# Performance work log

Hardware: AMD Instinct MI355X
Metric: run time of the kernel (lower is better)

Reference implementation:

```python
import jax, jax.numpy as jnp
import numpy as np
from jax import lax

A = 3          # anchors per scale
C = 80         # num foreground classes (COCO)
NMS_THRESH = 0.45
NMS_TOPK = 400
POST_NMS = 100


def setup_inputs() -> dict:
    key = jax.random.key(0)
    k0, k1, k2 = jax.random.split(key, 3)
    B = 8
    ch = A * (C + 5)  # 255
    # raw head outputs (pre-decode conv activations), modest scale so exp() stays sane
    tip0 = jax.random.normal(k0, (B, ch, 19, 19), jnp.float32) * 0.5
    tip1 = jax.random.normal(k1, (B, ch, 38, 38), jnp.float32) * 0.5
    tip2 = jax.random.normal(k2, (B, ch, 76, 76), jnp.float32) * 0.5
    # standard YOLOv3 COCO anchors, deepest scale (stride 32) first
    anchors0 = jnp.array([[116., 90.], [156., 198.], [373., 326.]], jnp.float32)
    anchors1 = jnp.array([[30., 61.], [62., 45.], [59., 119.]], jnp.float32)
    anchors2 = jnp.array([[10., 13.], [16., 30.], [33., 23.]], jnp.float32)
    return dict(tip0=tip0, tip1=tip1, tip2=tip2,
                anchors0=anchors0, anchors1=anchors1, anchors2=anchors2)


def _decode(tip, anchors, stride):
    """YOLOOutputV3 inference decode. tip: (B, A*(C+5), H, W)."""
    B, _, H, W = tip.shape
    # (B, A*(C+5), H*W) -> (B, H*W, A, C+5)
    pred = tip.reshape(B, A * (C + 5), H * W).transpose(0, 2, 1).reshape(B, H * W, A, C + 5)
    gx, gy = jnp.meshgrid(jnp.arange(W), jnp.arange(H))       # each (H, W)
    offsets = jnp.stack([gx, gy], -1).reshape(1, H * W, 1, 2).astype(tip.dtype)
    centers = (jax.nn.sigmoid(pred[..., :2]) + offsets) * stride          # (B,HW,A,2)
    scales = jnp.exp(pred[..., 2:4]) * anchors.reshape(1, 1, A, 2)        # (B,HW,A,2)
    conf = jax.nn.sigmoid(pred[..., 4:5])                                 # objectness
    cls_scores = jax.nn.sigmoid(pred[..., 5:]) * conf                      # (B,HW,A,C)
    wh = scales * 0.5
    bbox = jnp.concatenate([centers - wh, centers + wh], -1)               # corner format
    return bbox.reshape(B, H * W * A, 4), cls_scores.reshape(B, H * W * A, C)


def _pairwise_iou(b):
    """b: (K,4) corner boxes -> (K,K) IoU."""
    x1, y1, x2, y2 = b[:, 0], b[:, 1], b[:, 2], b[:, 3]
    area = jnp.maximum(x2 - x1, 0.) * jnp.maximum(y2 - y1, 0.)
    iw = jnp.maximum(jnp.minimum(x2[:, None], x2[None, :]) - jnp.maximum(x1[:, None], x1[None, :]), 0.)
    ih = jnp.maximum(jnp.minimum(y2[:, None], y2[None, :]) - jnp.maximum(y1[:, None], y1[None, :]), 0.)
    inter = iw * ih
    return inter / (area[:, None] + area[None, :] - inter + 1e-12)


def _nms_single(det):
    """Class-aware greedy NMS on one image. det: (M,6) = (cid, score, x1,y1,x2,y2)."""
    K = NMS_TOPK
    _, idx = lax.top_k(det[:, 1], K)     # sort by score, keep top K
    d = det[idx]                          # (K,6), descending score
    iou = _pairwise_iou(d[:, 2:6])
    same = d[:, 0][:, None] == d[:, 0][None, :]   # only same class suppresses
    valid = d[:, 1] > 0.
    rng = jnp.arange(K)

    def body(i, keep):
        sup = (iou[i] > NMS_THRESH) & same[i] & (rng > i) & keep[i] & valid[i]
        return keep & ~sup

    keep = lax.fori_loop(0, K, body, jnp.ones((K,), bool)) & valid
    d = jnp.where(keep[:, None], d, jnp.full_like(d, -1.))
    order = jnp.argsort(-d[:, 1])         # kept (sorted) first, suppressed (-1) last
    return d[order][:POST_NMS]            # (POST_NMS, 6)


def _detect(tip0, tip1, tip2, anchors0, anchors1, anchors2):
    dets = []
    for tip, anc, stride in ((tip0, anchors0, 32), (tip1, anchors1, 16), (tip2, anchors2, 8)):
        bbox, scores = _decode(tip, anc, stride)          # (B,N,4), (B,N,C)
        B, N, _ = bbox.shape
        ids = jnp.broadcast_to(jnp.arange(C, dtype=bbox.dtype)[None, None, :, None], (B, N, C, 1))
        sc = scores[..., None]                            # (B,N,C,1)
        bx = jnp.broadcast_to(bbox[:, :, None, :], (B, N, C, 4))
        dets.append(jnp.concatenate([ids, sc, bx], -1).reshape(B, N * C, 6))
    det = jnp.concatenate(dets, 1)                        # (B, M, 6)
    return jax.vmap(_nms_single)(det)                     # (B, POST_NMS, 6)


def reference(tip0, tip1, tip2, anchors0, anchors1, anchors2):
    res = _detect(tip0, tip1, tip2, anchors0, anchors1, anchors2)
    ids = res[..., 0:1]
    scores = res[..., 1:2]
    bboxes = res[..., 2:6]
    return ids, scores, bboxes
```

## Files before the change

### kernel.cpp

```cpp
#include <hip/hip_runtime.h>
#include <stdint.h>

#define NUMA 3
#define NUMC 80
#define CAP  49152
#define CAP2 8192
#define KTOP 400
#define POST 100
#define NBIN1 2048
#define EQCAP 1024
#define KEY0 0x3EE66666u
#define LBUF 2048

typedef float f32x4 __attribute__((ext_vector_type(4)));

__device__ __forceinline__ float sigmoidf_(float x) { return 1.0f / (1.0f + expf(-x)); }
__device__ __forceinline__ unsigned uminu(unsigned a, unsigned b) { return a < b ? a : b; }

__global__ void init_kernel(unsigned* __restrict__ p) {
    int i = blockIdx.x * blockDim.x + threadIdx.x;
    if (i < NBIN1 * 16 + 40) p[i] = 0;
}

__global__ __launch_bounds__(256) void score_main(
        const float* __restrict__ t0, const float* __restrict__ t1,
        const float* __restrict__ t2,
        unsigned* __restrict__ ccnt, unsigned* __restrict__ ckey,
        unsigned* __restrict__ cidx, unsigned* __restrict__ histN)
{
    __shared__ unsigned lkey[LBUF], lidx[LBUF];
    __shared__ unsigned lh[NBIN1];
    __shared__ unsigned lcnt, lbase;
    const int tid = threadIdx.x;
    if (tid == 0) lcnt = 0;
    for (int i = tid; i < NBIN1; i += 256) lh[i] = 0;
    __syncthreads();

    const int ba = blockIdx.z;
    const int b = ba / 3, a = ba - 3 * b;
    const int c0 = blockIdx.y * 8;
    const int cx = blockIdx.x;

    #define LEMIT(SC, IDX) do { \
        unsigned key_ = __float_as_uint(SC); \
        if (key_ >= KEY0) { \
            atomicAdd(&lh[(key_ - KEY0) >> 13], 1u); \
            unsigned pos_ = atomicAdd(&lcnt, 1u); \
            if (pos_ < LBUF) { lkey[pos_] = key_; lidx[pos_] = (IDX); } \
        } \
    } while (0)

    if (cx < 2) {
        const int hw = cx * 256 + tid;
        if (hw < 361) {
            const float* base = t0 + (size_t)(b * 255 + a * 85) * 361;
            float cr = base[4 * 361 + hw];
            const float* p0 = base + (size_t)(5 + c0) * 361 + hw;
            float x0 = p0[0 * 361], x1 = p0[1 * 361], x2 = p0[2 * 361], x3 = p0[3 * 361];
            float x4 = p0[4 * 361], x5 = p0[5 * 361], x6 = p0[6 * 361], x7 = p0[7 * 361];
            float cf = sigmoidf_(cr);
            unsigned ib = (unsigned)((hw * NUMA + a) * NUMC + c0);
            LEMIT(sigmoidf_(x0) * cf, ib + 0);
            LEMIT(sigmoidf_(x1) * cf, ib + 1);
            LEMIT(sigmoidf_(x2) * cf, ib + 2);
            LEMIT(sigmoidf_(x3) * cf, ib + 3);
            LEMIT(sigmoidf_(x4) * cf, ib + 4);
            LEMIT(sigmoidf_(x5) * cf, ib + 5);
            LEMIT(sigmoidf_(x6) * cf, ib + 6);
            LEMIT(sigmoidf_(x7) * cf, ib + 7);
        }
    } else {
        const float* tip; int vHW, v, candOff;
        if (cx < 4) { tip = t1; vHW = 361;  v = (cx - 2) * 256 + tid; candOff = 86640; }
        else        { tip = t2; vHW = 1444; v = (cx - 4) * 256 + tid; candOff = 433200; }
        if (v < vHW) {
            const f32x4* bp = (const f32x4*)(tip + (size_t)(b * 255 + a * 85) * (size_t)(vHW * 4));
            f32x4 cv = bp[(size_t)4 * vHW + v];
            const f32x4* p0 = bp + (size_t)(5 + c0) * vHW + v;
            f32x4 s0 = p0[0 * (size_t)vHW], s1 = p0[1 * (size_t)vHW];
            f32x4 s2 = p0[2 * (size_t)vHW], s3 = p0[3 * (size_t)vHW];
            f32x4 s4 = p0[4 * (size_t)vHW], s5 = p0[5 * (size_t)vHW];
            f32x4 s6 = p0[6 * (size_t)vHW], s7 = p0[7 * (size_t)vHW];
            float cf0 = sigmoidf_(cv[0]), cf1 = sigmoidf_(cv[1]);
            float cf2 = sigmoidf_(cv[2]), cf3 = sigmoidf_(cv[3]);
            unsigned ib0 = (unsigned)(candOff + (v * 4 * NUMA + a) * NUMC + c0);
            #define EMIT4(S, U) do { \
                unsigned ib = ib0 + (U); \
                LEMIT(sigmoidf_((S)[0]) * cf0, ib); \
                LEMIT(sigmoidf_((S)[1]) * cf1, ib + 240); \
                LEMIT(sigmoidf_((S)[2]) * cf2, ib + 480); \
                LEMIT(sigmoidf_((S)[3]) * cf3, ib + 720); \
            } while (0)
            EMIT4(s0, 0); EMIT4(s1, 1); EMIT4(s2, 2); EMIT4(s3, 3);
            EMIT4(s4, 4); EMIT4(s5, 5); EMIT4(s6, 6); EMIT4(s7, 7);
            #undef EMIT4
        }
    }
    #undef LEMIT

    __syncthreads();
    if (tid == 0) {
        unsigned c = lcnt;
        if (c > LBUF) {
            atomicOr(&ccnt[b], 0x80000000u);
            lbase = 0xFFFFFFFFu;
        } else {
            lbase = atomicAdd(&ccnt[b], c);
        }
    }
    __syncthreads();
    unsigned c = uminu(lcnt, (unsigned)LBUF);
    unsigned basep = lbase;
    if (basep != 0xFFFFFFFFu) {
        for (unsigned i = tid; i < c; i += 256) {
            unsigned p = basep + i;
            if (p < CAP) {
                ckey[(size_t)b * CAP + p] = lkey[i];
                cidx[(size_t)b * CAP + p] = lidx[i];
            }
        }
    }
    unsigned* gh = histN + b * NBIN1;
    for (int i = tid; i < NBIN1; i += 256) {
        unsigned v2 = lh[i];
        if (v2) atomicAdd(&gh[i], v2);
    }
}

__device__ __forceinline__ void wave_select(const unsigned* h, int nbins, unsigned rank,
                                            unsigned* resv, int tid)
{
    if (tid >= 64) return;
    const int lane = tid;
    const int cs = nbins >> 6;
    unsigned v = 0;
    for (int k = 0; k < cs; k++) {
        int off = (k + lane) & (cs - 1);
        v += h[lane * cs + off];
    }
    unsigned S = v;
    #pragma unroll
    for (int o = 1; o < 64; o <<= 1) {
        unsigned t = (unsigned)__shfl_down((int)S, o);
        if (lane + o < 64) S += t;
    }
    unsigned long long bm = __ballot(S >= rank);
    if (bm == 0ull) bm = 1ull;
    int C = 63 - __builtin_clzll(bm);
    unsigned SC = (unsigned)__builtin_amdgcn_readlane((int)S, C);
    unsigned vC = (unsigned)__builtin_amdgcn_readlane((int)v, C);
    unsigned rem = rank - (SC - vC);
    unsigned w = (lane < cs) ? h[C * cs + lane] : 0u;
    unsigned T = w;
    #pragma unroll
    for (int o = 1; o < 64; o <<= 1) {
        unsigned t = (unsigned)__shfl_down((int)T, o);
        if (lane + o < 64) T += t;
    }
    unsigned long long bm2 = __ballot((T >= rem) && (lane < cs));
    if (bm2 == 0ull) bm2 = 1ull;
    int B = 63 - __builtin_clzll(bm2);
    unsigned TB = (unsigned)__builtin_amdgcn_readlane((int)T, B);
    unsigned wB = (unsigned)__builtin_amdgcn_readlane((int)w, B);
    if (lane == 0) {
        resv[0] = (unsigned)(C * cs + B);
        resv[1] = rem - (TB - wB);
    }
}

__global__ __launch_bounds__(256) void findcut_v(const unsigned* __restrict__ histN,
                                                 unsigned* __restrict__ cutfloor,
                                                 unsigned* __restrict__ ccnt,
                                                 unsigned* __restrict__ flags) {
    __shared__ unsigned h[NBIN1];
    __shared__ unsigned resv[2];
    int b = blockIdx.x;
    for (int i = threadIdx.x; i < NBIN1; i += 256) h[i] = histN[b * NBIN1 + i];
    __syncthreads();
    wave_select(h, NBIN1, KTOP, resv, threadIdx.x);
    __syncthreads();
    if (threadIdx.x == 0) {
        unsigned c = ccnt[b];
        bool ok = (c >= KTOP) && (c <= CAP);
        flags[b] = ok ? 1u : 0u;
        if (ok) {
            cutfloor[b] = KEY0 + (resv[0] << 13);
        } else {
            cutfloor[b] = 0u;
            ccnt[b] = 0;
        }
    }
}

__global__ __launch_bounds__(256) void fb_hist(
        const float* __restrict__ t0, const float* __restrict__ t1,
        const float* __restrict__ t2,
        unsigned* __restrict__ histF, const unsigned* __restrict__ flags)
{
    const int ba = blockIdx.z;
    const int b = ba / 3, a = ba - 3 * b;
    if (flags[b]) return;
    __shared__ unsigned lh[NBIN1];
    const int tid = threadIdx.x;
    for (int i = tid; i < NBIN1; i += 256) lh[i] = 0;
    __syncthreads();
    const int c0 = blockIdx.y * 8;
    const int cx = blockIdx.x;
    if (cx < 2) {
        const int hw = cx * 256 + tid;
        if (hw < 361) {
            const float* base = t0 + (size_t)(b * 255 + a * 85) * 361;
            float cf = sigmoidf_(base[4 * 361 + hw]);
            for (int u = 0; u < 8; u++) {
                float sc = sigmoidf_(base[(size_t)(5 + c0 + u) * 361 + hw]) * cf;
                atomicAdd(&lh[__float_as_uint(sc) >> 19], 1u);
            }
        }
    } else {
        const float* tip; int vHW, v;
        if (cx < 4) { tip = t1; vHW = 361;  v = (cx - 2) * 256 + tid; }
        else        { tip = t2; vHW = 1444; v = (cx - 4) * 256 + tid; }
        if (v < vHW) {
            const f32x4* bp = (const f32x4*)(tip + (size_t)(b * 255 + a * 85) * (size_t)(vHW * 4));
            f32x4 cv = bp[(size_t)4 * vHW + v];
            float cf[4] = { sigmoidf_(cv[0]), sigmoidf_(cv[1]), sigmoidf_(cv[2]), sigmoidf_(cv[3]) };
            for (int u = 0; u < 8; u++) {
                f32x4 s = bp[(size_t)(5 + c0 + u) * vHW + v];
                for (int l = 0; l < 4; l++)
                    atomicAdd(&lh[__float_as_uint(sigmoidf_(s[l]) * cf[l]) >> 19], 1u);
            }
        }
    }
    __syncthreads();
    unsigned* gh = histF + b * NBIN1;
    for (int i = tid; i < NBIN1; i += 256) {
        unsigned v2 = lh[i];
        if (v2) atomicAdd(&gh[i], v2);
    }
}

__global__ __launch_bounds__(256) void fb_cut(const unsigned* __restrict__ histF,
                                              unsigned* __restrict__ cutb,
                                              const unsigned* __restrict__ flags) {
    int b = blockIdx.x;
    if (flags[b]) return;
    __shared__ unsigned h[NBIN1];
    __shared__ unsigned resv[2];
    for (int i = threadIdx.x; i < NBIN1; i += 256) h[i] = histF[b * NBIN1 + i];
    __syncthreads();
    wave_select(h, NBIN1, KTOP, resv, threadIdx.x);
    __syncthreads();
    if (threadIdx.x == 0) cutb[b] = resv[0];
}

__global__ __launch_bounds__(256) void fb_compact(
        const float* __restrict__ t0, const float* __restrict__ t1,
        const float* __restrict__ t2,
        const unsigned* __restrict__ cutb, unsigned* __restrict__ ccnt,
        unsigned* __restrict__ ckey, unsigned* __restrict__ cidx,
        const unsigned* __restrict__ flags)
{
    const int ba = blockIdx.z;
    const int b = ba / 3, a = ba - 3 * b;
    if (flags[b]) return;
    const int tid = threadIdx.x;
    const int c0 = blockIdx.y * 8;
    const int cx = blockIdx.x;
    unsigned cutkey = cutb[b] << 19;

    if (cx < 2) {
        const int hw = cx * 256 + tid;
        if (hw < 361) {
            const float* base = t0 + (size_t)(b * 255 + a * 85) * 361;
            float cf = sigmoidf_(base[4 * 361 + hw]);
            for (int u = 0; u < 8; u++) {
                float sc = sigmoidf_(base[(size_t)(5 + c0 + u) * 361 + hw]) * cf;
                unsigned key = __float_as_uint(sc);
                if (key >= cutkey) {
                    unsigned pos = atomicAdd(&ccnt[b], 1u);
                    if (pos < CAP) {
                        ckey[(size_t)b * CAP + pos] = key;
                        cidx[(size_t)b * CAP + pos] = (unsigned)((hw * NUMA + a) * NUMC + c0 + u);
                    }
                }
            }
        }
    } else {
        const float* tip; int vHW, v, candOff;
        if (cx < 4) { tip = t1; vHW = 361;  v = (cx - 2) * 256 + tid; candOff = 86640; }
        else        { tip = t2; vHW = 1444; v = (cx - 4) * 256 + tid; candOff = 433200; }
        if (v < vHW) {
            const f32x4* bp = (const f32x4*)(tip + (size_t)(b * 255 + a * 85) * (size_t)(vHW * 4));
            f32x4 cv = bp[(size_t)4 * vHW + v];
            float cf[4] = { sigmoidf_(cv[0]), sigmoidf_(cv[1]), sigmoidf_(cv[2]), sigmoidf_(cv[3]) };
            unsigned ib0 = (unsigned)(candOff + (v * 4 * NUMA + a) * NUMC + c0);
            for (int u = 0; u < 8; u++) {
                f32x4 s = bp[(size_t)(5 + c0 + u) * vHW + v];
                for (int l = 0; l < 4; l++) {
                    float sc = sigmoidf_(s[l]) * cf[l];
                    unsigned key = __float_as_uint(sc);
                    if (key >= cutkey) {
                        unsigned pos = atomicAdd(&ccnt[b], 1u);
                        if (pos < CAP) {
                            ckey[(size_t)b * CAP + pos] = key;
                            cidx[(size_t)b * CAP + pos] = ib0 + (unsigned)u + (unsigned)l * 240;
                        }
                    }
                }
            }
        }
    }
}

__global__ __launch_bounds__(256) void prefilter(
        const unsigned* __restrict__ ckey, const unsigned* __restrict__ cidx,
        const unsigned* __restrict__ ccnt, const unsigned* __restrict__ cutfloor,
        unsigned* __restrict__ cnt2, unsigned* __restrict__ ckey2,
        unsigned* __restrict__ cidx2)
{
    __shared__ unsigned lk[LBUF], li[LBUF];
    __shared__ unsigned lcnt, lbase;
    const int tid = threadIdx.x;
    const int b = blockIdx.z;
    if (tid == 0) lcnt = 0;
    __syncthreads();
    const unsigned n = uminu(ccnt[b], (unsigned)CAP);
    const unsigned cutf = cutfloor[b];
    const unsigned* ck = ckey + (size_t)b * CAP;
    const unsigned* ci = cidx + (size_t)b * CAP;
    for (unsigned i = blockIdx.x * 256 + tid; i < n; i += 32 * 256) {
        unsigned k = ck[i];
        if (k >= cutf) {
            unsigned p = atomicAdd(&lcnt, 1u);
            if (p < LBUF) { lk[p] = k; li[p] = ci[i]; }
        }
    }
    __syncthreads();
    if (tid == 0) lbase = atomicAdd(&cnt2[b], uminu(lcnt, (unsigned)LBUF));
    __syncthreads();
    unsigned c = uminu(lcnt, (unsigned)LBUF);
    for (unsigned i = tid; i < c; i += 256) {
        unsigned p = lbase + i;
        if (p < CAP2) {
            ckey2[(size_t)b * CAP2 + p] = lk[i];
            cidx2[(size_t)b * CAP2 + p] = li[i];
        }
    }
}

__global__ __launch_bounds__(512) void nms_kernel(
        const float* __restrict__ t0, const float* __restrict__ t1,
        const float* __restrict__ t2,
        const float* __restrict__ anc0, const float* __restrict__ anc1,
        const float* __restrict__ anc2,
        const unsigned* __restrict__ ckey, const unsigned* __restrict__ cidx,
        const unsigned* __restrict__ ccnt,
        const unsigned* __restrict__ ckey2, const unsigned* __restrict__ cidx2,
        const unsigned* __restrict__ cnt2, float* __restrict__ out)
{
    const int b = blockIdx.x;
    const int tid = threadIdx.x;
    const int T = 512;

    __shared__ unsigned hist[4096];
    __shared__ unsigned resv[2];
    __shared__ unsigned selk[512], seli[512];
    __shared__ unsigned eqi[EQCAP];
    __shared__ float sx1[KTOP], sy1[KTOP], sx2[KTOP], sy2[KTOP], ssc[KTOP];
    __shared__ int   scid[KTOP];
    __shared__ unsigned long long maskS[KTOP * 7];
    __shared__ unsigned long long vkeep[7];
    __shared__ unsigned cnts[2];
    __shared__ float oid[POST], osc[POST], obb[POST * 4];

    unsigned n2 = cnt2[b];
    const unsigned* ck; const unsigned* ci; unsigned n;
    if (n2 <= (unsigned)CAP2) {
        ck = ckey2 + (size_t)b * CAP2; ci = cidx2 + (size_t)b * CAP2; n = n2;
    } else {
        ck = ckey + (size_t)b * CAP; ci = cidx + (size_t)b * CAP;
        n = uminu(ccnt[b], (unsigned)CAP);
    }

    for (int i = tid; i < NBIN1; i += T) hist[i] = 0;
    __syncthreads();
    for (unsigned i = tid; i < n; i += T) atomicAdd(&hist[ck[i] >> 19], 1u);
    __syncthreads();
    wave_select(hist, NBIN1, KTOP, resv, tid);
    __syncthreads();
    unsigned b1 = resv[0], r2 = resv[1];
    __syncthreads();

    for (int i = tid; i < 4096; i += T) hist[i] = 0;
    __syncthreads();
    for (unsigned i = tid; i < n; i += T) {
        unsigned k = ck[i];
        if ((k >> 19) == b1) atomicAdd(&hist[(k >> 7) & 0xFFFu], 1u);
    }
    __syncthreads();
    wave_select(hist, 4096, r2, resv, tid);
    __syncthreads();
    unsigned b2 = resv[0], r3 = resv[1];
    __syncthreads();

    for (int i = tid; i < 128; i += T) hist[i] = 0;
    __syncthreads();
    unsigned pref = (b1 << 12) | b2;
    for (unsigned i = tid; i < n; i += T) {
        unsigned k = ck[i];
        if ((k >> 7) == pref) atomicAdd(&hist[k & 127u], 1u);
    }
    __syncthreads();
    wave_select(hist, 128, r3, resv, tid);
    __syncthreads();
    unsigned b3 = resv[0], needEq = resv[1];
    unsigned K400 = (b1 << 19) | (b2 << 7) | b3;
    __syncthreads();

    selk[tid] = 0u; seli[tid] = 0xFFFFFFFFu;
    for (int i = tid; i < EQCAP; i += T) eqi[i] = 0xFFFFFFFFu;
    if (tid == 0) { cnts[0] = 0; cnts[1] = 0; }
    __syncthreads();
    for (unsigned i = tid; i < n; i += T) {
        unsigned k = ck[i];
        if (k > K400) {
            unsigned p = atomicAdd(&cnts[0], 1u);
            if (p < KTOP) { selk[p] = k; seli[p] = ci[i]; }
        } else if (k == K400) {
            unsigned q = atomicAdd(&cnts[1], 1u);
            if (q < EQCAP) eqi[q] = ci[i];
        }
    }
    __syncthreads();
    unsigned selCnt = uminu(cnts[0], (unsigned)KTOP);
    unsigned eqN   = uminu(cnts[1], (unsigned)EQCAP);

    if (eqN > needEq) {
        int P2 = 1; while ((unsigned)P2 < eqN) P2 <<= 1;
        for (int k2 = 2; k2 <= P2; k2 <<= 1) {
            for (int j = k2 >> 1; j > 0; j >>= 1) {
                __syncthreads();
                for (int i = tid; i < P2; i += T) {
                    int ixj = i ^ j;
                    if (ixj > i && ixj < P2) {
                        unsigned va = eqi[i], vb = eqi[ixj];
                        bool up = ((i & k2) == 0);
                        if (up ? (va > vb) : (va < vb)) { eqi[i] = vb; eqi[ixj] = va; }
                    }
                }
            }
        }
        __syncthreads();
    }
    for (unsigned t2v = tid; t2v < needEq; t2v += T) {
        unsigned p = selCnt + t2v;
        if (p < KTOP) { selk[p] = K400; seli[p] = eqi[t2v]; }
    }
    __syncthreads();

    for (int k2 = 2; k2 <= 512; k2 <<= 1) {
        int j = k2 >> 1;
        for (; j >= 64; j >>= 1) {
            __syncthreads();
            int i = tid, ixj = i ^ j;
            if (ixj > i) {
                unsigned ka = selk[i], kb = selk[ixj], ia = seli[i], ib = seli[ixj];
                bool before = (ka > kb) || (ka == kb && ia < ib);
                bool up = ((i & k2) == 0);
                if (up ? !before : before) {
                    selk[i] = kb; selk[ixj] = ka; seli[i] = ib; seli[ixj] = ia;
                }
            }
        }
        __syncthreads();
        for (; j > 0; j >>= 1) {
            int i = tid, ixj = i ^ j;
            if (ixj > i) {
                unsigned ka = selk[i], kb = selk[ixj], ia = seli[i], ib = seli[ixj];
                bool before = (ka > kb) || (ka == kb && ia < ib);
                bool up = ((i & k2) == 0);
                if (up ? !before : before) {
                    selk[i] = kb; selk[ixj] = ka; seli[i] = ib; seli[ixj] = ia;
                }
            }
        }
    }
    __syncthreads();

    if (tid < KTOP) {
        unsigned idx = seli[tid];
        const float* tip; const float* anc; int HW, W, candOff; float strideF;
        if (idx < 86640u)       { tip = t0; anc = anc0; HW = 361;  W = 19; strideF = 32.f; candOff = 0; }
        else if (idx < 433200u) { tip = t1; anc = anc1; HW = 1444; W = 38; strideF = 16.f; candOff = 86640; }
        else                    { tip = t2; anc = anc2; HW = 5776; W = 76; strideF = 8.f;  candOff = 433200; }
        unsigned local = idx - (unsigned)candOff;
        int cls = (int)(local % NUMC);
        int nn  = (int)(local / NUMC);
        int a = nn % NUMA, hwl = nn / NUMA;
        const float* base = tip + (size_t)(b * 255 + a * 85) * HW + hwl;
        float tx = base[0];
        float ty = base[(size_t)HW];
        float tw = base[(size_t)2 * HW];
        float th = base[(size_t)3 * HW];
        float fx = (float)(hwl % W), fy = (float)(hwl / W);
        float cx = (sigmoidf_(tx) + fx) * strideF;
        float cy = (sigmoidf_(ty) + fy) * strideF;
        float hw_ = expf(tw) * anc[2 * a]     * 0.5f;
        float hh_ = expf(th) * anc[2 * a + 1] * 0.5f;
        sx1[tid] = cx - hw_; sy1[tid] = cy - hh_;
        sx2[tid] = cx + hw_; sy2[tid] = cy + hh_;
        ssc[tid] = __uint_as_float(selk[tid]);
        scid[tid] = cls;
    }
    __syncthreads();

    for (int p = tid; p < KTOP * 7; p += T) {
        int i = p / 7, w = p - i * 7;
        float x1i = sx1[i], y1i = sy1[i], x2i = sx2[i], y2i = sy2[i];
        float ai = fmaxf(x2i - x1i, 0.f) * fmaxf(y2i - y1i, 0.f);
        int cidI = scid[i];
        unsigned long long m = 0ull;
        int j0 = w * 64;
        int j1 = j0 + 64; if (j1 > KTOP) j1 = KTOP;
        int js = j0 > i + 1 ? j0 : i + 1;
        for (int j = js; j < j1; j++) {
            if (scid[j] != cidI) continue;
            float iw = fminf(x2i, sx2[j]) - fmaxf(x1i, sx1[j]);
            float ih = fminf(y2i, sy2[j]) - fmaxf(y1i, sy1[j]);
            iw = fmaxf(iw, 0.f); ih = fmaxf(ih, 0.f);
            float inter = iw * ih;
            float aj = fmaxf(sx2[j] - sx1[j], 0.f) * fmaxf(sy2[j] - sy1[j], 0.f);
            float iou = inter / (ai + aj - inter + 1e-12f);
            if (iou > 0.45f) m |= (1ull << (j - j0));
        }
        maskS[p] = m;
    }
    __syncthreads();

    if (tid < 64) {
        unsigned long long keep = 0ull;
        if (tid < 7) keep = (tid == 6) ? 0xFFFFull : ~0ull;
        unsigned long long m = (tid < 7) ? maskS[tid] : 0ull;
        for (int i = 0; i < KTOP; i++) {
            unsigned long long mn = (tid < 7 && i + 1 < KTOP) ? maskS[(i + 1) * 7 + tid] : 0ull;
            int w = i >> 6;
            unsigned klo = (unsigned)__builtin_amdgcn_readlane((int)(unsigned)(keep & 0xFFFFFFFFull), w);
            unsigned khi = (unsigned)__builtin_amdgcn_readlane((int)(unsigned)(keep >> 32), w);
            unsigned long long kw = ((unsigned long long)khi << 32) | klo;
            if ((kw >> (i & 63)) & 1ull) keep &= ~m;
            m = mn;
        }
        if (tid < 7) vkeep[tid] = keep;
    }
    __syncthreads();

    if (tid < POST) { oid[tid] = -1.f; osc[tid] = -1.f; }
    if (tid < POST * 4) obb[tid] = -1.f;
    __syncthreads();
    if (tid < KTOP) {
        int w = tid >> 6, bp = tid & 63;
        unsigned long long kw = vkeep[w];
        if ((kw >> bp) & 1ull) {
            int r = 0;
            for (int q = 0; q < w; q++) r += __popcll(vkeep[q]);
            r += __popcll(kw & ((1ull << bp) - 1ull));
            if (r < POST) {
                oid[r] = (float)scid[tid];
                osc[r] = ssc[tid];
                obb[r * 4 + 0] = sx1[tid];
                obb[r * 4 + 1] = sy1[tid];
                obb[r * 4 + 2] = sx2[tid];
                obb[r * 4 + 3] = sy2[tid];
            }
        }
    }
    __syncthreads();
    if (tid < POST) {
        out[b * POST + tid]       = oid[tid];
        out[800 + b * POST + tid] = osc[tid];
    }
    if (tid < POST * 4) out[1600 + b * POST * 4 + tid] = obb[tid];
}

extern "C" void kernel_launch(void* const* d_in, const int* in_sizes, int n_in,
                              void* d_out, int out_size, void* d_ws, size_t ws_size,
                              hipStream_t stream)
{
    const float* tip0 = (const float*)d_in[0];
    const float* tip1 = (const float*)d_in[1];
    const float* tip2 = (const float*)d_in[2];
    const float* anc0 = (const float*)d_in[3];
    const float* anc1 = (const float*)d_in[4];
    const float* anc2 = (const float*)d_in[5];
    float* out = (float*)d_out;

    unsigned* histN    = (unsigned*)d_ws;
    unsigned* histF    = histN + 8 * NBIN1;
    unsigned* cutb     = histF + 8 * NBIN1;
    unsigned* cutfloor = cutb + 8;
    unsigned* ccnt     = cutfloor + 8;
    unsigned* cnt2     = ccnt + 8;
    unsigned* flags    = cnt2 + 8;
    unsigned* ckey     = flags + 8;
    unsigned* cidx     = ckey + (size_t)8 * CAP;
    unsigned* ckey2    = cidx + (size_t)8 * CAP;
    unsigned* cidx2    = ckey2 + (size_t)8 * CAP2;

    init_kernel<<<(NBIN1 * 16 + 40 + 255) / 256, 256, 0, stream>>>(histN);

    dim3 g(10, 10, 24);
    score_main<<<g, 256, 0, stream>>>(tip0, tip1, tip2, ccnt, ckey, cidx, histN);
    findcut_v<<<8, 256, 0, stream>>>(histN, cutfloor, ccnt, flags);
    fb_hist<<<g, 256, 0, stream>>>(tip0, tip1, tip2, histF, flags);
    fb_cut<<<8, 256, 0, stream>>>(histF, cutb, flags);
    fb_compact<<<g, 256, 0, stream>>>(tip0, tip1, tip2, cutb, ccnt, ckey, cidx, flags);
    prefilter<<<dim3(32, 1, 8), 256, 0, stream>>>(ckey, cidx, ccnt, cutfloor,
                                                  cnt2, ckey2, cidx2);
    nms_kernel<<<8, 512, 0, stream>>>(tip0, tip1, tip2, anc0, anc1, anc2,
                                      ckey, cidx, ccnt, ckey2, cidx2, cnt2, out);
}
```

Baseline: 220.5 us.

## Split NMS into top-k, parallel IoU mask, and greedy-scan kernels

The single per-batch NMS kernel is split into three kernels. Top-k selection and box decode write to global scratch, a mask kernel computes the IoU suppression bitmask across many blocks instead of 8, and a greedy kernel runs the serial keep scan with an 8-deep unrolled prefetch of mask rows. This spreads the quadratic IoU work across the GPU. The cost is two extra launches and global round-trips for boxes and masks.

```diff
diff --git a/kernel.cpp b/kernel.cpp
--- a/kernel.cpp
+++ b/kernel.cpp
@@ -11,6 +11,7 @@
 #define EQCAP 1024
 #define KEY0 0x3EE66666u
 #define LBUF 2048
+#define NMASK (KTOP * 7)
 
 typedef float f32x4 __attribute__((ext_vector_type(4)));
 
@@ -348,7 +349,7 @@
     }
 }
 
-__global__ __launch_bounds__(512) void nms_kernel(
+__global__ __launch_bounds__(512) void topk_kernel(
         const float* __restrict__ t0, const float* __restrict__ t1,
         const float* __restrict__ t2,
         const float* __restrict__ anc0, const float* __restrict__ anc1,
@@ -356,7 +357,10 @@
         const unsigned* __restrict__ ckey, const unsigned* __restrict__ cidx,
         const unsigned* __restrict__ ccnt,
         const unsigned* __restrict__ ckey2, const unsigned* __restrict__ cidx2,
-        const unsigned* __restrict__ cnt2, float* __restrict__ out)
+        const unsigned* __restrict__ cnt2,
+        float* __restrict__ dX1, float* __restrict__ dY1,
+        float* __restrict__ dX2, float* __restrict__ dY2,
+        float* __restrict__ dSC, unsigned* __restrict__ dCID)
 {
     const int b = blockIdx.x;
     const int tid = threadIdx.x;
@@ -366,12 +370,7 @@
     __shared__ unsigned resv[2];
     __shared__ unsigned selk[512], seli[512];
     __shared__ unsigned eqi[EQCAP];
-    __shared__ float sx1[KTOP], sy1[KTOP], sx2[KTOP], sy2[KTOP], ssc[KTOP];
-    __shared__ int   scid[KTOP];
-    __shared__ unsigned long long maskS[KTOP * 7];
-    __shared__ unsigned long long vkeep[7];
     __shared__ unsigned cnts[2];
-    __shared__ float oid[POST], osc[POST], obb[POST * 4];
 
     unsigned n2 = cnt2[b];
     const unsigned* ck; const unsigned* ci; unsigned n;
@@ -507,56 +506,97 @@
         float cy = (sigmoidf_(ty) + fy) * strideF;
         float hw_ = expf(tw) * anc[2 * a]     * 0.5f;
         float hh_ = expf(th) * anc[2 * a + 1] * 0.5f;
-        sx1[tid] = cx - hw_; sy1[tid] = cy - hh_;
-        sx2[tid] = cx + hw_; sy2[tid] = cy + hh_;
-        ssc[tid] = __uint_as_float(selk[tid]);
-        scid[tid] = cls;
-    }
-    __syncthreads();
-
-    for (int p = tid; p < KTOP * 7; p += T) {
+        int o = b * KTOP + tid;
+        dX1[o] = cx - hw_; dY1[o] = cy - hh_;
+        dX2[o] = cx + hw_; dY2[o] = cy + hh_;
+        dSC[o] = __uint_as_float(selk[tid]);
+        dCID[o] = (unsigned)cls;
+    }
+}
+
+__global__ __launch_bounds__(256) void mask_kernel(
+        const float* __restrict__ dX1, const float* __restrict__ dY1,
+        const float* __restrict__ dX2, const float* __restrict__ dY2,
+        const unsigned* __restrict__ dCID, unsigned long long* __restrict__ maskG)
+{
+    __shared__ float lx1[KTOP], ly1[KTOP], lx2[KTOP], ly2[KTOP];
+    __shared__ int lcid[KTOP];
+    const int b = blockIdx.y;
+    const int tid = threadIdx.x;
+    for (int i = tid; i < KTOP; i += 256) {
+        int o = b * KTOP + i;
+        lx1[i] = dX1[o]; ly1[i] = dY1[o];
+        lx2[i] = dX2[o]; ly2[i] = dY2[o];
+        lcid[i] = (int)dCID[o];
+    }
+    __syncthreads();
+    int p = blockIdx.x * 256 + tid;
+    if (p < NMASK) {
         int i = p / 7, w = p - i * 7;
-        float x1i = sx1[i], y1i = sy1[i], x2i = sx2[i], y2i = sy2[i];
+        float x1i = lx1[i], y1i = ly1[i], x2i = lx2[i], y2i = ly2[i];
         float ai = fmaxf(x2i - x1i, 0.f) * fmaxf(y2i - y1i, 0.f);
-        int cidI = scid[i];
+        int cidI = lcid[i];
         unsigned long long m = 0ull;
         int j0 = w * 64;
         int j1 = j0 + 64; if (j1 > KTOP) j1 = KTOP;
         int js = j0 > i + 1 ? j0 : i + 1;
         for (int j = js; j < j1; j++) {
-            if (scid[j] != cidI) continue;
-            float iw = fminf(x2i, sx2[j]) - fmaxf(x1i, sx1[j]);
-            float ih = fminf(y2i, sy2[j]) - fmaxf(y1i, sy1[j]);
+            if (lcid[j] != cidI) continue;
+            float iw = fminf(x2i, lx2[j]) - fmaxf(x1i, lx1[j]);
+            float ih = fminf(y2i, ly2[j]) - fmaxf(y1i, ly1[j]);
             iw = fmaxf(iw, 0.f); ih = fmaxf(ih, 0.f);
             float inter = iw * ih;
-            float aj = fmaxf(sx2[j] - sx1[j], 0.f) * fmaxf(sy2[j] - sy1[j], 0.f);
+            float aj = fmaxf(lx2[j] - lx1[j], 0.f) * fmaxf(ly2[j] - ly1[j], 0.f);
             float iou = inter / (ai + aj - inter + 1e-12f);
             if (iou > 0.45f) m |= (1ull << (j - j0));
         }
-        maskS[p] = m;
-    }
-    __syncthreads();
-
-    if (tid < 64) {
-        unsigned long long keep = 0ull;
-        if (tid < 7) keep = (tid == 6) ? 0xFFFFull : ~0ull;
-        unsigned long long m = (tid < 7) ? maskS[tid] : 0ull;
-        for (int i = 0; i < KTOP; i++) {
-            unsigned long long mn = (tid < 7 && i + 1 < KTOP) ? maskS[(i + 1) * 7 + tid] : 0ull;
-            int w = i >> 6;
-            unsigned klo = (unsigned)__builtin_amdgcn_readlane((int)(unsigned)(keep & 0xFFFFFFFFull), w);
-            unsigned khi = (unsigned)__builtin_amdgcn_readlane((int)(unsigned)(keep >> 32), w);
-            unsigned long long kw = ((unsigned long long)khi << 32) | klo;
-            if ((kw >> (i & 63)) & 1ull) keep &= ~m;
-            m = mn;
-        }
-        if (tid < 7) vkeep[tid] = keep;
-    }
-    __syncthreads();
-
+        maskG[(size_t)b * NMASK + p] = m;
+    }
+}
+
+__global__ __launch_bounds__(512) void greedy_kernel(
+        const float* __restrict__ dX1, const float* __restrict__ dY1,
+        const float* __restrict__ dX2, const float* __restrict__ dY2,
+        const float* __restrict__ dSC, const unsigned* __restrict__ dCID,
+        const unsigned long long* __restrict__ maskG, float* __restrict__ out)
+{
+    __shared__ unsigned long long maskL[NMASK];
+    __shared__ unsigned long long vkeep[7];
+    __shared__ float oid[POST], osc[POST], obb[POST * 4];
+    const int b = blockIdx.x;
+    const int tid = threadIdx.x;
+
+    for (int i = tid; i < NMASK; i += 512) maskL[i] = maskG[(size_t)b * NMASK + i];
     if (tid < POST) { oid[tid] = -1.f; osc[tid] = -1.f; }
     if (tid < POST * 4) obb[tid] = -1.f;
     __syncthreads();
+
+    if (tid < 64) {
+        const int lane = tid;
+        unsigned long long keep = 0ull;
+        if (lane < 7) keep = (lane == 6) ? 0xFFFFull : ~0ull;
+        unsigned long long mb[8];
+        #pragma unroll
+        for (int k = 0; k < 8; k++)
+            mb[k] = (lane < 7) ? maskL[k * 7 + lane] : 0ull;
+        for (int ib = 0; ib < KTOP; ib += 8) {
+            #pragma unroll
+            for (int k = 0; k < 8; k++) {
+                int i = ib + k;
+                unsigned long long m = mb[k];
+                int nf = ib + 8 + k;
+                mb[k] = (lane < 7 && nf < KTOP) ? maskL[nf * 7 + lane] : 0ull;
+                int w = i >> 6;
+                unsigned klo = (unsigned)__builtin_amdgcn_readlane((int)(unsigned)(keep & 0xFFFFFFFFull), w);
+                unsigned khi = (unsigned)__builtin_amdgcn_readlane((int)(unsigned)(keep >> 32), w);
+                unsigned long long kw = ((unsigned long long)khi << 32) | klo;
+                if ((kw >> (i & 63)) & 1ull) keep &= ~m;
+            }
+        }
+        if (lane < 7) vkeep[lane] = keep;
+    }
+    __syncthreads();
+
     if (tid < KTOP) {
         int w = tid >> 6, bp = tid & 63;
         unsigned long long kw = vkeep[w];
@@ -565,12 +605,13 @@
             for (int q = 0; q < w; q++) r += __popcll(vkeep[q]);
             r += __popcll(kw & ((1ull << bp) - 1ull));
             if (r < POST) {
-                oid[r] = (float)scid[tid];
-                osc[r] = ssc[tid];
-                obb[r * 4 + 0] = sx1[tid];
-                obb[r * 4 + 1] = sy1[tid];
-                obb[r * 4 + 2] = sx2[tid];
-                obb[r * 4 + 3] = sy2[tid];
+                int o = b * KTOP + tid;
+                oid[r] = (float)(int)dCID[o];
+                osc[r] = dSC[o];
+                obb[r * 4 + 0] = dX1[o];
+                obb[r * 4 + 1] = dY1[o];
+                obb[r * 4 + 2] = dX2[o];
+                obb[r * 4 + 3] = dY2[o];
             }
         }
     }
@@ -605,6 +646,13 @@
     unsigned* cidx     = ckey + (size_t)8 * CAP;
     unsigned* ckey2    = cidx + (size_t)8 * CAP;
     unsigned* cidx2    = ckey2 + (size_t)8 * CAP2;
+    float*    dX1      = (float*)(cidx2 + (size_t)8 * CAP2);
+    float*    dY1      = dX1 + 8 * KTOP;
+    float*    dX2      = dY1 + 8 * KTOP;
+    float*    dY2      = dX2 + 8 * KTOP;
+    float*    dSC      = dY2 + 8 * KTOP;
+    unsigned* dCID     = (unsigned*)(dSC + 8 * KTOP);
+    unsigned long long* maskG = (unsigned long long*)(dCID + 8 * KTOP);
 
     init_kernel<<<(NBIN1 * 16 + 40 + 255) / 256, 256, 0, stream>>>(histN);
 
@@ -616,6 +664,10 @@
     fb_compact<<<g, 256, 0, stream>>>(tip0, tip1, tip2, cutb, ccnt, ckey, cidx, flags);
     prefilter<<<dim3(32, 1, 8), 256, 0, stream>>>(ckey, cidx, ccnt, cutfloor,
                                                   cnt2, ckey2, cidx2);
-    nms_kernel<<<8, 512, 0, stream>>>(tip0, tip1, tip2, anc0, anc1, anc2,
-                                      ckey, cidx, ccnt, ckey2, cidx2, cnt2, out);
-}
+    topk_kernel<<<8, 512, 0, stream>>>(tip0, tip1, tip2, anc0, anc1, anc2,
+                                       ckey, cidx, ccnt, ckey2, cidx2, cnt2,
+                                       dX1, dY1, dX2, dY2, dSC, dCID);
+    mask_kernel<<<dim3((NMASK + 255) / 256, 8), 256, 0, stream>>>(
+        dX1, dY1, dX2, dY2, dCID, maskG);
+    greedy_kernel<<<8, 512, 0, stream>>>(dX1, dY1, dX2, dY2, dSC, dCID, maskG, out);
+}
```

After: 195.9 us. 11.2% less time.
